# Kernel tuning notes

Measured on AMD Instinct MI355X. Metric: run time of the kernel, lower is better.

The kernel has to match this reference:

```python
import jax, jax.numpy as jnp
import numpy as np

N, E, D = 50000, 512000, 128

def mish(x):
    return x * jnp.tanh(jax.nn.softplus(x))

def ln(x, g, b):
    m = jnp.mean(x, axis=-1, keepdims=True)
    v = jnp.var(x, axis=-1, keepdims=True)
    return (x - m) / jnp.sqrt(v + 1e-5) * g + b

def setup_inputs():
    key = jax.random.key(0)
    ks = jax.random.split(key, 16)
    W = lambda k, i, o: jax.random.normal(k, (i, o), jnp.float32) * 0.02
    z = jnp.zeros((D,), jnp.float32)
    o = jnp.ones((D,), jnp.float32)
    return {
        "node_feat": jax.random.normal(ks[0], (N, D), jnp.float32),
        "coord_feat": jax.random.normal(ks[1], (N, D), jnp.float32),
        "Wq": W(ks[2], D, D), "bq": z, "gq": o, "beq": z,
        "Wk": W(ks[3], D, D), "bk": z, "gk": o, "bek": z,
        "Wm1": W(ks[4], D, D), "bm1": z, "gm": o, "bem": z,
        "Wm2": W(ks[5], D, D), "bm2": z,
        "Wb1": W(ks[6], D, D), "bb1": z, "gb": o, "beb": z,
        "Wb2": W(ks[7], D, D), "bb2": z,
        "Ww1": W(ks[8], D, D), "bw1": z, "gw": o, "bew": z,
        "Ww2": W(ks[9], D, D), "bw2": z,
        "Wn1": W(ks[10], 2 * D, D), "bn1": z,
        "Wn2": W(ks[11], D, D), "bn2": z,
        "Wc1": W(ks[12], D, D), "bc1": z,
        "Wc2": W(ks[13], D, D),
        "src": jax.random.randint(ks[14], (E,), 0, N, jnp.int32),
        "dst": jax.random.randint(ks[15], (E,), 0, N, jnp.int32),
    }

def reference(node_feat, coord_feat, Wq, bq, gq, beq, Wk, bk, gk, bek,
              Wm1, bm1, gm, bem, Wm2, bm2, Wb1, bb1, gb, beb, Wb2, bb2,
              Ww1, bw1, gw, bew, Ww2, bw2, Wn1, bn1, Wn2, bn2, Wc1, bc1, Wc2,
              src, dst):
    # linear_q / linear_k on coord features: Linear -> LayerNorm -> Mish
    q = mish(ln(coord_feat @ Wq + bq, gq, beq))   # [N, D]
    k = mish(ln(coord_feat @ Wk + bk, gk, bek))   # [N, D]
    # u_sub_v('q','k'): per-edge q[src] - k[dst]
    rel = q[src] - k[dst]                          # [E, D]
    radial = jnp.sum(rel * rel, axis=-1, keepdims=True)  # [E, 1]
    rel = rel / jnp.sqrt(radial + 1e-8)
    # relative position encodings from dst coord features
    xd = coord_feat[dst]                           # [E, D]
    pem = mish(ln(xd @ Wm1 + bm1, gm, bem)) @ Wm2 + bm2
    peb = mish(ln(xd @ Wb1 + bb1, gb, beb)) @ Wb2 + bb2
    rel = rel * pem + peb
    # weight_encoding MLP
    w = mish(ln(rel @ Ww1 + bw1, gw, bew)) @ Ww2 + bw2  # [E, D]
    # dgl.softmax_edges over a single graph: softmax across the edge axis
    w = jax.nn.softmax(w, axis=0)
    # update_all(copy_e, sum): scatter-add edge weights to destination nodes
    h_neigh = jax.ops.segment_sum(w, dst, num_segments=N)  # [N, D]
    h = mish(jnp.concatenate([node_feat, h_neigh], axis=-1) @ Wn1 + bn1) @ Wn2 + bn2
    x = mish(coord_feat @ Wc1 + bc1) @ Wc2
    return (h, x)
```

## Files before the change

kernel.cpp:

```cpp
#include <hip/hip_runtime.h>
#include <cstdint>
#include <cstddef>

#define DN 128
#define NND 50000
#define NED 512000
#define NSCAN 49

typedef __attribute__((ext_vector_type(8))) short bf8;
typedef __attribute__((ext_vector_type(4))) float f4;
typedef unsigned short us;

__device__ __forceinline__ us f2bf(float f){
  union { float f; unsigned int u; } c; c.f = f;
  unsigned int r = c.u + 0x7fffu + ((c.u >> 16) & 1u);
  return (us)(r >> 16);
}
__device__ __forceinline__ float bf2f(us u){
  union { unsigned int u; float f; } c; c.u = ((unsigned int)u) << 16;
  return c.f;
}
__device__ __forceinline__ float mishf(float x){
  float e = __expf(x);
  float u = 1.f + e;
  float u2 = u * u;
  float t = (u2 - 1.f) / (u2 + 1.f);
  return x * ((x > 20.f) ? 1.f : t);
}

#define MFMA16(a, b, c) __builtin_amdgcn_mfma_f32_16x16x32_bf16((a), (b), (c), 0, 0, 0)

__device__ __forceinline__ bf8 lds_frag(const us* base, int row, int rowStrideB, int kElem){
  int byte = row * rowStrideB + kElem * 2;
  byte ^= (row & 7) << 4;
  return *(const bf8*)((const char*)base + byte);
}
__device__ __forceinline__ bf8 gfrag(const us* W, int n, int K, int kElem){
  return *(const bf8*)(W + (size_t)n * K + kElem);
}

template<int OUT_BF16>
__device__ __forceinline__ void store_tile(void* outp, int nrows, int r0,
                                           int wr, int wc, int g, int s, int ostride,
                                           const f4 (&A)[2][4]){
#pragma unroll
  for (int rt = 0; rt < 2; ++rt)
#pragma unroll
    for (int ct = 0; ct < 4; ++ct)
#pragma unroll
      for (int reg = 0; reg < 4; ++reg){
        int row = r0 + wr*32 + rt*16 + g*4 + reg;
        if (row < nrows){
          int col = wc*64 + ct*16 + s;
          float v = A[rt][ct][reg];
          if constexpr (OUT_BF16 != 0)
            ((us*)outp)[(size_t)row*ostride + col] = f2bf(v);
          else
            ((float*)outp)[(size_t)row*ostride + col] = v;
        }
      }
}

__device__ __forceinline__ void gemm_reg(const bf8 (&a)[2][4], const us* __restrict__ WT,
                                         const float* __restrict__ bias,
                                         int wc, int g, int s, f4 (&acc)[2][4]){
#pragma unroll
  for (int ct = 0; ct < 4; ++ct){
    float bv = bias ? bias[wc*64 + ct*16 + s] : 0.f;
    f4 t = {bv, bv, bv, bv};
    acc[0][ct] = t; acc[1][ct] = t;
  }
#pragma unroll
  for (int ct = 0; ct < 4; ++ct){
    int n = wc*64 + ct*16 + s;
#pragma unroll
    for (int kk = 0; kk < 4; ++kk){
      bf8 b = gfrag(WT, n, DN, kk*32 + g*8);
      acc[0][ct] = MFMA16(a[0][kk], b, acc[0][ct]);
      acc[1][ct] = MFMA16(a[1][kk], b, acc[1][ct]);
    }
  }
}

__device__ __forceinline__ void ln_mish(f4 (&acc)[2][4],
                                        const float* __restrict__ gam,
                                        const float* __restrict__ bet,
                                        int wr, int wc, int g, int s,
                                        float (*rowsum)[64][2], float (*rowsq)[64][2],
                                        int buf){
  float gv[4], bev[4];
#pragma unroll
  for (int ct = 0; ct < 4; ++ct){ int n = wc*64 + ct*16 + s; gv[ct] = gam[n]; bev[ct] = bet[n]; }
#pragma unroll
  for (int rt = 0; rt < 2; ++rt)
#pragma unroll
    for (int reg = 0; reg < 4; ++reg){
      float sm = acc[rt][0][reg] + acc[rt][1][reg] + acc[rt][2][reg] + acc[rt][3][reg];
      float sq = acc[rt][0][reg]*acc[rt][0][reg] + acc[rt][1][reg]*acc[rt][1][reg]
               + acc[rt][2][reg]*acc[rt][2][reg] + acc[rt][3][reg]*acc[rt][3][reg];
#pragma unroll
      for (int m = 1; m < 16; m <<= 1){ sm += __shfl_xor(sm, m, 64); sq += __shfl_xor(sq, m, 64); }
      if (s == 0){
        int row = wr*32 + rt*16 + g*4 + reg;
        rowsum[buf][row][wc] = sm; rowsq[buf][row][wc] = sq;
      }
    }
  __syncthreads();
#pragma unroll
  for (int rt = 0; rt < 2; ++rt)
#pragma unroll
    for (int reg = 0; reg < 4; ++reg){
      int row = wr*32 + rt*16 + g*4 + reg;
      float sm = rowsum[buf][row][0] + rowsum[buf][row][1];
      float sq = rowsq[buf][row][0] + rowsq[buf][row][1];
      float mu = sm * (1.f/128.f);
      float var = sq * (1.f/128.f) - mu*mu;
      float rs = rsqrtf(var + 1e-5f);
#pragma unroll
      for (int ct = 0; ct < 4; ++ct)
        acc[rt][ct][reg] = mishf((acc[rt][ct][reg] - mu) * rs * gv[ct] + bev[ct]);
    }
}

__device__ __forceinline__ void write_T(us* Tsh, int wr, int wc, int g, int s,
                                        const f4 (&A)[2][4]){
#pragma unroll
  for (int rt = 0; rt < 2; ++rt)
#pragma unroll
    for (int ct = 0; ct < 4; ++ct)
#pragma unroll
      for (int reg = 0; reg < 4; ++reg){
        int row = wr*32 + rt*16 + g*4 + reg;
        int col = wc*64 + ct*16 + s;
        int byte = row*256 + col*2; byte ^= (row & 7) << 4;
        *(us*)((char*)Tsh + byte) = f2bf(A[rt][ct][reg]);
      }
}

__device__ __forceinline__ void load_a2(const us* Tsh, int wr, int g, int s, bf8 (&a2)[2][4]){
#pragma unroll
  for (int rt = 0; rt < 2; ++rt)
#pragma unroll
    for (int kk = 0; kk < 4; ++kk)
      a2[rt][kk] = lds_frag(Tsh, wr*32 + rt*16 + s, 256, kk*32 + g*8);
}

__global__ __launch_bounds__(256, 2)
void node_fused(const float* __restrict__ X,
                const us* __restrict__ WqT,  const float* __restrict__ bq,
                const float* __restrict__ gq, const float* __restrict__ beq,
                const us* __restrict__ WkT,  const float* __restrict__ bk,
                const float* __restrict__ gk, const float* __restrict__ bek,
                const us* __restrict__ Wm1T, const float* __restrict__ bm1,
                const float* __restrict__ gm, const float* __restrict__ bem,
                const us* __restrict__ Wm2T, const float* __restrict__ bm2,
                const us* __restrict__ Wb1T, const float* __restrict__ bb1,
                const float* __restrict__ gb, const float* __restrict__ beb,
                const us* __restrict__ Wb2T, const float* __restrict__ bb2,
                const us* __restrict__ Wc1T, const float* __restrict__ bc1,
                const us* __restrict__ Wc2T,
                us* __restrict__ qt, us* __restrict__ kmb, float* __restrict__ xout)
{
  __shared__ us Ash[64 * DN];
  __shared__ float rowsum[2][64][2];
  __shared__ float rowsq[2][64][2];

  const int tid = threadIdx.x;
  const int r0 = blockIdx.x * 64;

  {
    int r = tid >> 2, c4 = tid & 3;
    int grow = r0 + r; if (grow >= NND) grow = NND - 1;
    const f4* sp = (const f4*)(X + (size_t)grow * DN + c4 * 32);
#pragma unroll
    for (int j = 0; j < 4; ++j){
      f4 v0 = sp[2*j], v1 = sp[2*j+1];
      bf8 o;
#pragma unroll
      for (int q = 0; q < 4; ++q){ o[q] = (short)f2bf(v0[q]); o[4+q] = (short)f2bf(v1[q]); }
      int byte = r*256 + c4*64 + j*16; byte ^= (r & 7) << 4;
      *(bf8*)((char*)Ash + byte) = o;
    }
  }
  __syncthreads();

  const int lane = tid & 63, w = tid >> 6;
  const int wr = w >> 1, wc = w & 1;
  const int g = lane >> 4, s = lane & 15;

  bf8 a[2][4];
#pragma unroll
  for (int rt = 0; rt < 2; ++rt)
#pragma unroll
    for (int kk = 0; kk < 4; ++kk)
      a[rt][kk] = lds_frag(Ash, wr*32 + rt*16 + s, 256, kk*32 + g*8);
  __syncthreads();

  f4 acc[2][4], acc2[2][4];
  bf8 a2[2][4];

  gemm_reg(a, WqT, bq, wc, g, s, acc);
  ln_mish(acc, gq, beq, wr, wc, g, s, rowsum, rowsq, 0);
  store_tile<1>((void*)qt, NND, r0, wr, wc, g, s, DN, acc);

  gemm_reg(a, WkT, bk, wc, g, s, acc);
  ln_mish(acc, gk, bek, wr, wc, g, s, rowsum, rowsq, 1);
  store_tile<1>((void*)kmb, NND, r0, wr, wc, g, s, 384, acc);

  gemm_reg(a, Wm1T, bm1, wc, g, s, acc);
  ln_mish(acc, gm, bem, wr, wc, g, s, rowsum, rowsq, 0);
  write_T(Ash, wr, wc, g, s, acc);
  __syncthreads();
  load_a2(Ash, wr, g, s, a2);
#pragma unroll
  for (int ct = 0; ct < 4; ++ct){
    float bv = bm2[wc*64 + ct*16 + s]; f4 t = {bv,bv,bv,bv}; acc2[0][ct] = t; acc2[1][ct] = t;
  }
#pragma unroll
  for (int ct = 0; ct < 4; ++ct){
    int n = wc*64 + ct*16 + s;
#pragma unroll
    for (int kk = 0; kk < 4; ++kk){
      bf8 b = gfrag(Wm2T, n, DN, kk*32 + g*8);
      acc2[0][ct] = MFMA16(a2[0][kk], b, acc2[0][ct]);
      acc2[1][ct] = MFMA16(a2[1][kk], b, acc2[1][ct]);
    }
  }
  store_tile<1>((void*)(kmb + 128), NND, r0, wr, wc, g, s, 384, acc2);

  gemm_reg(a, Wb1T, bb1, wc, g, s, acc);
  ln_mish(acc, gb, beb, wr, wc, g, s, rowsum, rowsq, 1);
  write_T(Ash, wr, wc, g, s, acc);
  __syncthreads();
  load_a2(Ash, wr, g, s, a2);
#pragma unroll
  for (int ct = 0; ct < 4; ++ct){
    float bv = bb2[wc*64 + ct*16 + s]; f4 t = {bv,bv,bv,bv}; acc2[0][ct] = t; acc2[1][ct] = t;
  }
#pragma unroll
  for (int ct = 0; ct < 4; ++ct){
    int n = wc*64 + ct*16 + s;
#pragma unroll
    for (int kk = 0; kk < 4; ++kk){
      bf8 b = gfrag(Wb2T, n, DN, kk*32 + g*8);
      acc2[0][ct] = MFMA16(a2[0][kk], b, acc2[0][ct]);
      acc2[1][ct] = MFMA16(a2[1][kk], b, acc2[1][ct]);
    }
  }
  store_tile<1>((void*)(kmb + 256), NND, r0, wr, wc, g, s, 384, acc2);

  gemm_reg(a, Wc1T, bc1, wc, g, s, acc);
#pragma unroll
  for (int rt = 0; rt < 2; ++rt)
#pragma unroll
    for (int ct = 0; ct < 4; ++ct)
#pragma unroll
      for (int reg = 0; reg < 4; ++reg)
        acc[rt][ct][reg] = mishf(acc[rt][ct][reg]);
  __syncthreads();
  write_T(Ash, wr, wc, g, s, acc);
  __syncthreads();
  load_a2(Ash, wr, g, s, a2);
#pragma unroll
  for (int ct = 0; ct < 4; ++ct){ f4 t = {0,0,0,0}; acc2[0][ct] = t; acc2[1][ct] = t; }
#pragma unroll
  for (int ct = 0; ct < 4; ++ct){
    int n = wc*64 + ct*16 + s;
#pragma unroll
    for (int kk = 0; kk < 4; ++kk){
      bf8 b = gfrag(Wc2T, n, DN, kk*32 + g*8);
      acc2[0][ct] = MFMA16(a2[0][kk], b, acc2[0][ct]);
      acc2[1][ct] = MFMA16(a2[1][kk], b, acc2[1][ct]);
    }
  }
  store_tile<0>((void*)xout, NND, r0, wr, wc, g, s, DN, acc2);
}

__global__ void csr_count(const int* __restrict__ dst, int* __restrict__ deg){
  int e = blockIdx.x * 256 + threadIdx.x;
  if (e < NED) atomicAdd(&deg[dst[e]], 1);
}

__global__ __launch_bounds__(1024) void csr_blocksum(const int* __restrict__ deg,
                                                     int* __restrict__ bsum){
  __shared__ int sb[1024];
  int t = threadIdx.x, idx = blockIdx.x * 1024 + t;
  sb[t] = (idx < NND) ? deg[idx] : 0;
  __syncthreads();
  for (int off = 512; off > 0; off >>= 1){
    if (t < off) sb[t] += sb[t + off];
    __syncthreads();
  }
  if (t == 0) bsum[blockIdx.x] = sb[0];
}

__global__ void csr_scanroot(const int* __restrict__ bsum, int* __restrict__ boff){
  if (threadIdx.x == 0){
    int run = 0;
    for (int b = 0; b < NSCAN; ++b){ boff[b] = run; run += bsum[b]; }
  }
}

__global__ __launch_bounds__(1024) void csr_scatter(const int* __restrict__ deg,
                                                    const int* __restrict__ boff,
                                                    int* __restrict__ fillctr){
  __shared__ int ss[1024];
  int t = threadIdx.x, idx = blockIdx.x * 1024 + t;
  int v = (idx < NND) ? deg[idx] : 0;
  ss[t] = v;
  __syncthreads();
  for (int off = 1; off < 1024; off <<= 1){
    int x = (t >= off) ? ss[t - off] : 0;
    __syncthreads();
    ss[t] += x;
    __syncthreads();
  }
  if (idx < NND){
    int p = boff[blockIdx.x] + ss[t] - v;
    fillctr[idx] = p;
  }
}

__global__ void csr_fill(const int* __restrict__ src, const int* __restrict__ dst,
                         int* __restrict__ fillctr,
                         int* __restrict__ ssorted, int* __restrict__ dsorted){
  int e = blockIdx.x * 256 + threadIdx.x;
  if (e < NED){
    int d = dst[e];
    int p = atomicAdd(&fillctr[d], 1);
    ssorted[p] = src[e];
    dsorted[p] = d;
  }
}

__global__ __launch_bounds__(256, 2)
void edge_kernel(const us* __restrict__ qtab,
                 const us* __restrict__ kmb,
                 const us* __restrict__ W1T,
                 const us* __restrict__ W2T,
                 const float* __restrict__ bw1,
                 const float* __restrict__ gwp,
                 const float* __restrict__ bewp,
                 const float* __restrict__ bw2,
                 const int* __restrict__ ssorted,
                 const int* __restrict__ dsorted,
                 float* __restrict__ hacc,
                 float* __restrict__ colsum8)
{
  __shared__ us Ash[64 * DN];
  __shared__ float rowsum[1][64][2];
  __shared__ float rowsq[1][64][2];
  __shared__ int dsh[64];

  const int tid = threadIdx.x;
  const int nchunk = gridDim.x >> 3;
  const int swz = (blockIdx.x & 7) * nchunk + (blockIdx.x >> 3);
  const int e0 = swz * 64;
  const int lane = tid & 63, w = tid >> 6;
  const int wr = w >> 1, wc = w & 1;
  const int g = lane >> 4, s = lane & 15;

  if (tid < 64) dsh[tid] = dsorted[e0 + tid];

  bf8 B1[4][4], B2[4][4];
  float b1v[4], gv[4], bev[4], b2v[4];
#pragma unroll
  for (int ct = 0; ct < 4; ++ct){
    int n = wc*64 + ct*16 + s;
#pragma unroll
    for (int kk = 0; kk < 4; ++kk){
      B1[ct][kk] = gfrag(W1T, n, DN, kk*32 + g*8);
      B2[ct][kk] = gfrag(W2T, n, DN, kk*32 + g*8);
    }
    b1v[ct] = bw1[n]; gv[ct] = gwp[n]; bev[ct] = bewp[n]; b2v[ct] = bw2[n];
  }

  {
    int r = tid >> 2, c4 = tid & 3;
    int e = e0 + r;
    int sn = ssorted[e], dn = dsorted[e];
    const bf8* qp = (const bf8*)(qtab + (size_t)sn * DN + c4 * 32);
    const us* kb = kmb + (size_t)dn * 384 + c4 * 32;
    float rel[32]; float ss = 0.f;
#pragma unroll
    for (int j = 0; j < 4; ++j){
      bf8 qv = qp[j];
      bf8 kv = *(const bf8*)(kb + j*8);
#pragma unroll
      for (int q = 0; q < 8; ++q){
        float d = bf2f((us)qv[q]) - bf2f((us)kv[q]);
        rel[j*8+q] = d; ss += d * d;
      }
    }
    ss += __shfl_xor(ss, 1, 64);
    ss += __shfl_xor(ss, 2, 64);
    float rinv = rsqrtf(ss + 1e-8f);
#pragma unroll
    for (int j = 0; j < 4; ++j){
      bf8 mv = *(const bf8*)(kb + 128 + j*8);
      bf8 bv = *(const bf8*)(kb + 256 + j*8);
      bf8 o;
#pragma unroll
      for (int q = 0; q < 8; ++q){
        float v = rel[j*8+q] * rinv * bf2f((us)mv[q]) + bf2f((us)bv[q]);
        o[q] = (short)f2bf(v);
      }
      int byte = r*256 + c4*64 + j*16; byte ^= (r & 7) << 4;
      *(bf8*)((char*)Ash + byte) = o;
    }
  }
  __syncthreads();

  f4 acc[2][4];
#pragma unroll
  for (int ct = 0; ct < 4; ++ct){ f4 t = {b1v[ct], b1v[ct], b1v[ct], b1v[ct]}; acc[0][ct] = t; acc[1][ct] = t; }
  bf8 a[2][4];
#pragma unroll
  for (int rt = 0; rt < 2; ++rt)
#pragma unroll
    for (int kk = 0; kk < 4; ++kk)
      a[rt][kk] = lds_frag(Ash, wr*32 + rt*16 + s, 256, kk*32 + g*8);
#pragma unroll
  for (int ct = 0; ct < 4; ++ct)
#pragma unroll
    for (int kk = 0; kk < 4; ++kk){
      acc[0][ct] = MFMA16(a[0][kk], B1[ct][kk], acc[0][ct]);
      acc[1][ct] = MFMA16(a[1][kk], B1[ct][kk], acc[1][ct]);
    }

#pragma unroll
  for (int rt = 0; rt < 2; ++rt)
#pragma unroll
    for (int reg = 0; reg < 4; ++reg){
      float sm = acc[rt][0][reg] + acc[rt][1][reg] + acc[rt][2][reg] + acc[rt][3][reg];
      float sq = acc[rt][0][reg]*acc[rt][0][reg] + acc[rt][1][reg]*acc[rt][1][reg]
               + acc[rt][2][reg]*acc[rt][2][reg] + acc[rt][3][reg]*acc[rt][3][reg];
#pragma unroll
      for (int m = 1; m < 16; m <<= 1){ sm += __shfl_xor(sm, m, 64); sq += __shfl_xor(sq, m, 64); }
      if (s == 0){
        int row = wr*32 + rt*16 + g*4 + reg;
        rowsum[0][row][wc] = sm; rowsq[0][row][wc] = sq;
      }
    }
  __syncthreads();
#pragma unroll
  for (int rt = 0; rt < 2; ++rt)
#pragma unroll
    for (int reg = 0; reg < 4; ++reg){
      int row = wr*32 + rt*16 + g*4 + reg;
      float sm = rowsum[0][row][0] + rowsum[0][row][1];
      float sq = rowsq[0][row][0] + rowsq[0][row][1];
      float mu = sm * (1.f/128.f);
      float var = sq * (1.f/128.f) - mu*mu;
      float rs = rsqrtf(var + 1e-5f);
#pragma unroll
      for (int ct = 0; ct < 4; ++ct)
        acc[rt][ct][reg] = mishf((acc[rt][ct][reg] - mu) * rs * gv[ct] + bev[ct]);
    }

  write_T(Ash, wr, wc, g, s, acc);
  __syncthreads();

  f4 p[2][4];
#pragma unroll
  for (int ct = 0; ct < 4; ++ct){ f4 t = {b2v[ct], b2v[ct], b2v[ct], b2v[ct]}; p[0][ct] = t; p[1][ct] = t; }
  bf8 a2[2][4];
  load_a2(Ash, wr, g, s, a2);
#pragma unroll
  for (int ct = 0; ct < 4; ++ct)
#pragma unroll
    for (int kk = 0; kk < 4; ++kk){
      p[0][ct] = MFMA16(a2[0][kk], B2[ct][kk], p[0][ct]);
      p[1][ct] = MFMA16(a2[1][kk], B2[ct][kk], p[1][ct]);
    }
#pragma unroll
  for (int rt = 0; rt < 2; ++rt)
#pragma unroll
    for (int ct = 0; ct < 4; ++ct)
#pragma unroll
      for (int reg = 0; reg < 4; ++reg)
        p[rt][ct][reg] = __expf(p[rt][ct][reg]);

  __syncthreads();

  write_T(Ash, wr, wc, g, s, p);
  __syncthreads();

  {
    int col = tid & 127, half = tid >> 7;
    int rbeg = half * 32;
    float csum = 0.f;
    int prev = dsh[rbeg];
    float run = 0.f;
#pragma unroll 8
    for (int r = rbeg; r < rbeg + 32; ++r){
      int d = dsh[r];
      int byte = r*256 + col*2; byte ^= (r & 7) << 4;
      float v = bf2f(*(const us*)((const char*)Ash + byte));
      csum += v;
      if (d != prev){
        atomicAdd(&hacc[(size_t)prev * DN + col], run);
        run = v; prev = d;
      } else {
        run += v;
      }
    }
    atomicAdd(&hacc[(size_t)prev * DN + col], run);
    atomicAdd(&colsum8[(blockIdx.x & 7) * DN + col], csum);
  }
}

__global__ __launch_bounds__(256, 2)
void final_h(const float* __restrict__ nodef,
             const float* __restrict__ hacc,
             const float* __restrict__ colsum8,
             const us* __restrict__ Wn1T,
             const float* __restrict__ bn1,
             const us* __restrict__ Wn2T,
             const float* __restrict__ bn2,
             float* __restrict__ outh)
{
  __shared__ us Ash[64 * 256];
  __shared__ float rcs[DN];

  const int tid = threadIdx.x;
  const int r0 = blockIdx.x * 64;

  if (tid < DN){
    float ssum = 0.f;
#pragma unroll
    for (int x = 0; x < 8; ++x) ssum += colsum8[x * DN + tid];
    rcs[tid] = 1.f / ssum;
  }
  __syncthreads();

  {
    int r = tid >> 2, c4 = tid & 3;
    int grow = r0 + r; if (grow >= NND) grow = NND - 1;
    const f4* np = (const f4*)(nodef + (size_t)grow * DN + c4 * 32);
    const f4* hp = (const f4*)(hacc + (size_t)grow * DN + c4 * 32);
#pragma unroll
    for (int j = 0; j < 4; ++j){
      f4 v0 = np[2*j], v1 = np[2*j+1];
      bf8 o;
#pragma unroll
      for (int q = 0; q < 4; ++q){ o[q] = (short)f2bf(v0[q]); o[4+q] = (short)f2bf(v1[q]); }
      int byte = r*512 + c4*64 + j*16; byte ^= (r & 7) << 4;
      *(bf8*)((char*)Ash + byte) = o;
      f4 h0 = hp[2*j], h1 = hp[2*j+1];
      bf8 o2;
#pragma unroll
      for (int q = 0; q < 4; ++q){
        o2[q]   = (short)f2bf(h0[q] * rcs[c4*32 + j*8 + q]);
        o2[4+q] = (short)f2bf(h1[q] * rcs[c4*32 + j*8 + 4 + q]);
      }
      int byte2 = r*512 + 256 + c4*64 + j*16; byte2 ^= (r & 7) << 4;
      *(bf8*)((char*)Ash + byte2) = o2;
    }
  }
  __syncthreads();

  const int lane = tid & 63, w = tid >> 6;
  const int wr = w >> 1, wc = w & 1;
  const int g = lane >> 4, s = lane & 15;

  float b1v[4], b2v[4];
#pragma unroll
  for (int ct = 0; ct < 4; ++ct){ int n = wc*64 + ct*16 + s; b1v[ct] = bn1[n]; b2v[ct] = bn2[n]; }

  f4 acc[2][4];
#pragma unroll
  for (int ct = 0; ct < 4; ++ct){ f4 t = {b1v[ct], b1v[ct], b1v[ct], b1v[ct]}; acc[0][ct] = t; acc[1][ct] = t; }

  bf8 a[2][8];
#pragma unroll
  for (int rt = 0; rt < 2; ++rt)
#pragma unroll
    for (int kk = 0; kk < 8; ++kk)
      a[rt][kk] = lds_frag(Ash, wr*32 + rt*16 + s, 512, kk*32 + g*8);
  __syncthreads();

#pragma unroll
  for (int ct = 0; ct < 4; ++ct){
    int n = wc*64 + ct*16 + s;
#pragma unroll
    for (int kk = 0; kk < 8; ++kk){
      bf8 b = gfrag(Wn1T, n, 256, kk*32 + g*8);
      acc[0][ct] = MFMA16(a[0][kk], b, acc[0][ct]);
      acc[1][ct] = MFMA16(a[1][kk], b, acc[1][ct]);
    }
  }

#pragma unroll
  for (int rt = 0; rt < 2; ++rt)
#pragma unroll
    for (int ct = 0; ct < 4; ++ct)
#pragma unroll
      for (int reg = 0; reg < 4; ++reg)
        acc[rt][ct][reg] = mishf(acc[rt][ct][reg]);
  write_T((us*)Ash, wr, wc, g, s, acc);
  __syncthreads();

  f4 acc2[2][4];
#pragma unroll
  for (int ct = 0; ct < 4; ++ct){ f4 t = {b2v[ct], b2v[ct], b2v[ct], b2v[ct]}; acc2[0][ct] = t; acc2[1][ct] = t; }
  bf8 a2[2][4];
  load_a2((const us*)Ash, wr, g, s, a2);
#pragma unroll
  for (int ct = 0; ct < 4; ++ct){
    int n = wc*64 + ct*16 + s;
#pragma unroll
    for (int kk = 0; kk < 4; ++kk){
      bf8 b = gfrag(Wn2T, n, DN, kk*32 + g*8);
      acc2[0][ct] = MFMA16(a2[0][kk], b, acc2[0][ct]);
      acc2[1][ct] = MFMA16(a2[1][kk], b, acc2[1][ct]);
    }
  }
  store_tile<0>((void*)outh, NND, r0, wr, wc, g, s, DN, acc2);
}

struct WPrepArgs {
  const float* w[12];
  us* wt[12];
  int K[12];
};

__global__ void prep_weights(WPrepArgs a){
  int widx = blockIdx.y;
  int K = a.K[widx];
  int idx = blockIdx.x * 256 + threadIdx.x;
  if (idx >= DN * K) return;
  int kshift = (K == 256) ? 8 : 7;
  int n = idx >> kshift;
  int k = idx & (K - 1);
  a.wt[widx][idx] = f2bf(a.w[widx][(size_t)k * DN + n]);
}

extern "C" void kernel_launch(void* const* d_in, const int* in_sizes, int n_in,
                              void* d_out, int out_size, void* d_ws, size_t ws_size,
                              hipStream_t stream) {
  const float* node_feat = (const float*)d_in[0];
  const float* coordf    = (const float*)d_in[1];
  const float* Wq  = (const float*)d_in[2];
  const float* bq  = (const float*)d_in[3];
  const float* gq  = (const float*)d_in[4];
  const float* beq = (const float*)d_in[5];
  const float* Wk  = (const float*)d_in[6];
  const float* bk  = (const float*)d_in[7];
  const float* gk  = (const float*)d_in[8];
  const float* bek = (const float*)d_in[9];
  const float* Wm1 = (const float*)d_in[10];
  const float* bm1 = (const float*)d_in[11];
  const float* gm  = (const float*)d_in[12];
  const float* bem = (const float*)d_in[13];
  const float* Wm2 = (const float*)d_in[14];
  const float* bm2 = (const float*)d_in[15];
  const float* Wb1 = (const float*)d_in[16];
  const float* bb1 = (const float*)d_in[17];
  const float* gb  = (const float*)d_in[18];
  const float* beb = (const float*)d_in[19];
  const float* Wb2 = (const float*)d_in[20];
  const float* bb2 = (const float*)d_in[21];
  const float* Ww1 = (const float*)d_in[22];
  const float* bw1 = (const float*)d_in[23];
  const float* gw  = (const float*)d_in[24];
  const float* bew = (const float*)d_in[25];
  const float* Ww2 = (const float*)d_in[26];
  const float* bw2 = (const float*)d_in[27];
  const float* Wn1 = (const float*)d_in[28];
  const float* bn1 = (const float*)d_in[29];
  const float* Wn2 = (const float*)d_in[30];
  const float* bn2 = (const float*)d_in[31];
  const float* Wc1 = (const float*)d_in[32];
  const float* bc1 = (const float*)d_in[33];
  const float* Wc2 = (const float*)d_in[34];
  const int* srcI  = (const int*)d_in[35];
  const int* dstI  = (const int*)d_in[36];

  char* ws = (char*)d_ws;
  size_t off = 0;
  auto alloc = [&](size_t bytes) -> char* {
    char* p = ws + off;
    off += (bytes + 255) & ~(size_t)255;
    return p;
  };
  us*    qt      = (us*)alloc((size_t)NND * DN * 2);
  us*    kmb     = (us*)alloc((size_t)NND * 384 * 2);
  float* hacc    = (float*)alloc((size_t)NND * DN * 4);
  float* colsum8 = (float*)alloc(8 * DN * 4);
  int*   deg     = (int*)alloc((size_t)NND * 4);
  int*   fillctr = (int*)alloc((size_t)NND * 4);
  int*   ssorted = (int*)alloc((size_t)NED * 4);
  int*   dsorted = (int*)alloc((size_t)NED * 4);
  int*   bsum    = (int*)alloc((size_t)NSCAN * 4);
  int*   boff    = (int*)alloc((size_t)NSCAN * 4);
  us*    wtb     = (us*)alloc((size_t)12 * 16384 * 2);

  hipMemsetAsync(hacc, 0, (size_t)NND * DN * 4 + 8 * DN * 4, stream);
  hipMemsetAsync(deg, 0, (size_t)NND * 4, stream);

  WPrepArgs pa;
  const float* wsrc[12] = {Wq, Wk, Wm1, Wm2, Wb1, Wb2, Ww1, Ww2, Wc1, Wc2, Wn2, Wn1};
  for (int i = 0; i < 12; ++i){
    pa.w[i] = wsrc[i];
    pa.wt[i] = wtb + (size_t)i * 16384;
    pa.K[i] = (i == 11) ? 256 : 128;
  }
  prep_weights<<<dim3(128, 12), 256, 0, stream>>>(pa);

  csr_count<<<(NED + 255) / 256, 256, 0, stream>>>(dstI, deg);
  csr_blocksum<<<NSCAN, 1024, 0, stream>>>(deg, bsum);
  csr_scanroot<<<1, 64, 0, stream>>>(bsum, boff);
  csr_scatter<<<NSCAN, 1024, 0, stream>>>(deg, boff, fillctr);
  csr_fill<<<(NED + 255) / 256, 256, 0, stream>>>(srcI, dstI, fillctr, ssorted, dsorted);

  const int NB = (NND + 63) / 64;

  node_fused<<<NB, 256, 0, stream>>>(coordf,
      pa.wt[0], bq, gq, beq,
      pa.wt[1], bk, gk, bek,
      pa.wt[2], bm1, gm, bem, pa.wt[3], bm2,
      pa.wt[4], bb1, gb, beb, pa.wt[5], bb2,
      pa.wt[8], bc1, pa.wt[9],
      qt, kmb, (float*)d_out + (size_t)NND * DN);

  edge_kernel<<<NED / 64, 256, 0, stream>>>(qt, kmb, pa.wt[6], pa.wt[7],
                                            bw1, gw, bew, bw2, ssorted, dsorted,
                                            hacc, colsum8);

  final_h<<<NB, 256, 0, stream>>>(node_feat, hacc, colsum8,
                                  pa.wt[11], bn1, pa.wt[10], bn2, (float*)d_out);
}
```

Measured before the change: 517.1 us.

## Give each warp its own 16-edge tile to drop block-wide syncs in edge kernel

The edge kernel is restructured so each of the four waves handles 16 edges end to end, with full 128-column GEMMs, a per-wave LayerNorm via shuffles, and a private LDS tile. This removes the cross-wave row-statistics exchange and most __syncthreads barriers. Weight fragments are now streamed from global/L2 inside the GEMM rather than preloaded into registers, which trades register pressure for repeated weight loads per wave. The gathers for q, k, pem and peb are also issued up front to overlap memory latency.

```diff
diff --git a/kernel.cpp b/kernel.cpp
--- a/kernel.cpp
+++ b/kernel.cpp
@@ -143,6 +143,65 @@
 #pragma unroll
     for (int kk = 0; kk < 4; ++kk)
       a2[rt][kk] = lds_frag(Tsh, wr*32 + rt*16 + s, 256, kk*32 + g*8);
+}
+
+__device__ __forceinline__ void loadA16(const us* T, int g, int s, bf8 (&a)[4]){
+#pragma unroll
+  for (int kk = 0; kk < 4; ++kk)
+    a[kk] = lds_frag(T, s, 256, kk*32 + g*8);
+}
+
+__device__ __forceinline__ void gemm8(const bf8 (&a)[4], const us* __restrict__ WT,
+                                      const float* __restrict__ bias,
+                                      int g, int s, f4 (&acc)[8]){
+#pragma unroll
+  for (int ct = 0; ct < 8; ++ct){
+    float bv = bias ? bias[ct*16 + s] : 0.f;
+    f4 t = {bv, bv, bv, bv};
+    acc[ct] = t;
+  }
+#pragma unroll
+  for (int ct = 0; ct < 8; ++ct){
+    int n = ct*16 + s;
+#pragma unroll
+    for (int kk = 0; kk < 4; ++kk)
+      acc[ct] = MFMA16(a[kk], gfrag(WT, n, DN, kk*32 + g*8), acc[ct]);
+  }
+}
+
+__device__ __forceinline__ void ln_mish8(f4 (&acc)[8],
+                                         const float* __restrict__ gam,
+                                         const float* __restrict__ bet, int s){
+  float mu[4], rs[4];
+#pragma unroll
+  for (int reg = 0; reg < 4; ++reg){
+    float sm = 0.f, sq = 0.f;
+#pragma unroll
+    for (int ct = 0; ct < 8; ++ct){ float v = acc[ct][reg]; sm += v; sq += v*v; }
+#pragma unroll
+    for (int m = 1; m < 16; m <<= 1){ sm += __shfl_xor(sm, m, 64); sq += __shfl_xor(sq, m, 64); }
+    float mm = sm * (1.f/128.f);
+    float var = sq * (1.f/128.f) - mm*mm;
+    mu[reg] = mm; rs[reg] = rsqrtf(var + 1e-5f);
+  }
+#pragma unroll
+  for (int ct = 0; ct < 8; ++ct){
+    float gv = gam[ct*16 + s], bv = bet[ct*16 + s];
+#pragma unroll
+    for (int reg = 0; reg < 4; ++reg)
+      acc[ct][reg] = mishf((acc[ct][reg] - mu[reg]) * rs[reg] * gv + bv);
+  }
+}
+
+__device__ __forceinline__ void writeT16(us* T, int g, int s, const f4 (&A)[8]){
+#pragma unroll
+  for (int ct = 0; ct < 8; ++ct)
+#pragma unroll
+    for (int reg = 0; reg < 4; ++reg){
+      int row = g*4 + reg, col = ct*16 + s;
+      int byte = row*256 + col*2; byte ^= (row & 7) << 4;
+      *(us*)((char*)T + byte) = f2bf(A[ct][reg]);
+    }
 }
 
 __global__ __launch_bounds__(256, 2)
@@ -347,143 +406,75 @@
                  float* __restrict__ hacc,
                  float* __restrict__ colsum8)
 {
-  __shared__ us Ash[64 * DN];
-  __shared__ float rowsum[1][64][2];
-  __shared__ float rowsq[1][64][2];
+  __shared__ us Tsh[4][16 * DN];
   __shared__ int dsh[64];
 
   const int tid = threadIdx.x;
+  const int lane = tid & 63, w = tid >> 6;
+  const int g = lane >> 4, s = lane & 15;
+  const int r = lane >> 2, c4 = lane & 3;
+
   const int nchunk = gridDim.x >> 3;
   const int swz = (blockIdx.x & 7) * nchunk + (blockIdx.x >> 3);
-  const int e0 = swz * 64;
-  const int lane = tid & 63, w = tid >> 6;
-  const int wr = w >> 1, wc = w & 1;
-  const int g = lane >> 4, s = lane & 15;
-
-  if (tid < 64) dsh[tid] = dsorted[e0 + tid];
-
-  bf8 B1[4][4], B2[4][4];
-  float b1v[4], gv[4], bev[4], b2v[4];
-#pragma unroll
-  for (int ct = 0; ct < 4; ++ct){
-    int n = wc*64 + ct*16 + s;
-#pragma unroll
-    for (int kk = 0; kk < 4; ++kk){
-      B1[ct][kk] = gfrag(W1T, n, DN, kk*32 + g*8);
-      B2[ct][kk] = gfrag(W2T, n, DN, kk*32 + g*8);
-    }
-    b1v[ct] = bw1[n]; gv[ct] = gwp[n]; bev[ct] = bewp[n]; b2v[ct] = bw2[n];
-  }
-
-  {
-    int r = tid >> 2, c4 = tid & 3;
-    int e = e0 + r;
-    int sn = ssorted[e], dn = dsorted[e];
-    const bf8* qp = (const bf8*)(qtab + (size_t)sn * DN + c4 * 32);
-    const us* kb = kmb + (size_t)dn * 384 + c4 * 32;
-    float rel[32]; float ss = 0.f;
-#pragma unroll
-    for (int j = 0; j < 4; ++j){
-      bf8 qv = qp[j];
-      bf8 kv = *(const bf8*)(kb + j*8);
-#pragma unroll
-      for (int q = 0; q < 8; ++q){
-        float d = bf2f((us)qv[q]) - bf2f((us)kv[q]);
-        rel[j*8+q] = d; ss += d * d;
-      }
-    }
-    ss += __shfl_xor(ss, 1, 64);
-    ss += __shfl_xor(ss, 2, 64);
-    float rinv = rsqrtf(ss + 1e-8f);
-#pragma unroll
-    for (int j = 0; j < 4; ++j){
-      bf8 mv = *(const bf8*)(kb + 128 + j*8);
-      bf8 bv = *(const bf8*)(kb + 256 + j*8);
-      bf8 o;
-#pragma unroll
-      for (int q = 0; q < 8; ++q){
-        float v = rel[j*8+q] * rinv * bf2f((us)mv[q]) + bf2f((us)bv[q]);
-        o[q] = (short)f2bf(v);
-      }
-      int byte = r*256 + c4*64 + j*16; byte ^= (r & 7) << 4;
-      *(bf8*)((char*)Ash + byte) = o;
-    }
-  }
-  __syncthreads();
-
-  f4 acc[2][4];
-#pragma unroll
-  for (int ct = 0; ct < 4; ++ct){ f4 t = {b1v[ct], b1v[ct], b1v[ct], b1v[ct]}; acc[0][ct] = t; acc[1][ct] = t; }
-  bf8 a[2][4];
-#pragma unroll
-  for (int rt = 0; rt < 2; ++rt)
-#pragma unroll
-    for (int kk = 0; kk < 4; ++kk)
-      a[rt][kk] = lds_frag(Ash, wr*32 + rt*16 + s, 256, kk*32 + g*8);
-#pragma unroll
-  for (int ct = 0; ct < 4; ++ct)
-#pragma unroll
-    for (int kk = 0; kk < 4; ++kk){
-      acc[0][ct] = MFMA16(a[0][kk], B1[ct][kk], acc[0][ct]);
-      acc[1][ct] = MFMA16(a[1][kk], B1[ct][kk], acc[1][ct]);
-    }
-
-#pragma unroll
-  for (int rt = 0; rt < 2; ++rt)
-#pragma unroll
-    for (int reg = 0; reg < 4; ++reg){
-      float sm = acc[rt][0][reg] + acc[rt][1][reg] + acc[rt][2][reg] + acc[rt][3][reg];
-      float sq = acc[rt][0][reg]*acc[rt][0][reg] + acc[rt][1][reg]*acc[rt][1][reg]
-               + acc[rt][2][reg]*acc[rt][2][reg] + acc[rt][3][reg]*acc[rt][3][reg];
-#pragma unroll
-      for (int m = 1; m < 16; m <<= 1){ sm += __shfl_xor(sm, m, 64); sq += __shfl_xor(sq, m, 64); }
-      if (s == 0){
-        int row = wr*32 + rt*16 + g*4 + reg;
-        rowsum[0][row][wc] = sm; rowsq[0][row][wc] = sq;
-      }
-    }
-  __syncthreads();
-#pragma unroll
-  for (int rt = 0; rt < 2; ++rt)
-#pragma unroll
-    for (int reg = 0; reg < 4; ++reg){
-      int row = wr*32 + rt*16 + g*4 + reg;
-      float sm = rowsum[0][row][0] + rowsum[0][row][1];
-      float sq = rowsq[0][row][0] + rowsq[0][row][1];
-      float mu = sm * (1.f/128.f);
-      float var = sq * (1.f/128.f) - mu*mu;
-      float rs = rsqrtf(var + 1e-5f);
-#pragma unroll
-      for (int ct = 0; ct < 4; ++ct)
-        acc[rt][ct][reg] = mishf((acc[rt][ct][reg] - mu) * rs * gv[ct] + bev[ct]);
-    }
-
-  write_T(Ash, wr, wc, g, s, acc);
-  __syncthreads();
-
-  f4 p[2][4];
-#pragma unroll
-  for (int ct = 0; ct < 4; ++ct){ f4 t = {b2v[ct], b2v[ct], b2v[ct], b2v[ct]}; p[0][ct] = t; p[1][ct] = t; }
-  bf8 a2[2][4];
-  load_a2(Ash, wr, g, s, a2);
-#pragma unroll
-  for (int ct = 0; ct < 4; ++ct)
-#pragma unroll
-    for (int kk = 0; kk < 4; ++kk){
-      p[0][ct] = MFMA16(a2[0][kk], B2[ct][kk], p[0][ct]);
-      p[1][ct] = MFMA16(a2[1][kk], B2[ct][kk], p[1][ct]);
-    }
-#pragma unroll
-  for (int rt = 0; rt < 2; ++rt)
-#pragma unroll
-    for (int ct = 0; ct < 4; ++ct)
-#pragma unroll
-      for (int reg = 0; reg < 4; ++reg)
-        p[rt][ct][reg] = __expf(p[rt][ct][reg]);
-
-  __syncthreads();
-
-  write_T(Ash, wr, wc, g, s, p);
+  const int e0 = swz * 64 + w * 16;
+  us* T = (us*)Tsh[w];
+
+  const int e = e0 + r;
+  const int sn = ssorted[e], dn = dsorted[e];
+  const bf8* qp = (const bf8*)(qtab + (size_t)sn * DN + c4 * 32);
+  const us*  kb = kmb + (size_t)dn * 384 + c4 * 32;
+  bf8 qv[4], kv[4], mv[4], bv[4];
+#pragma unroll
+  for (int j = 0; j < 4; ++j){
+    qv[j] = qp[j];
+    kv[j] = *(const bf8*)(kb + j*8);
+    mv[j] = *(const bf8*)(kb + 128 + j*8);
+    bv[j] = *(const bf8*)(kb + 256 + j*8);
+  }
+  if (c4 == 0) dsh[w*16 + r] = dn;
+
+  float ss = 0.f;
+#pragma unroll
+  for (int j = 0; j < 4; ++j)
+#pragma unroll
+    for (int q = 0; q < 8; ++q){
+      float d = bf2f((us)qv[j][q]) - bf2f((us)kv[j][q]);
+      ss += d * d;
+    }
+  ss += __shfl_xor(ss, 1, 64);
+  ss += __shfl_xor(ss, 2, 64);
+  float rinv = rsqrtf(ss + 1e-8f);
+
+#pragma unroll
+  for (int j = 0; j < 4; ++j){
+    bf8 o;
+#pragma unroll
+    for (int q = 0; q < 8; ++q){
+      float d = bf2f((us)qv[j][q]) - bf2f((us)kv[j][q]);
+      float v = d * rinv * bf2f((us)mv[j][q]) + bf2f((us)bv[j][q]);
+      o[q] = (short)f2bf(v);
+    }
+    int byte = r*256 + c4*64 + j*16; byte ^= (r & 7) << 4;
+    *(bf8*)((char*)T + byte) = o;
+  }
+
+  bf8 a[4];
+  loadA16(T, g, s, a);
+  f4 acc[8];
+  gemm8(a, W1T, bw1, g, s, acc);
+  ln_mish8(acc, gwp, bewp, s);
+  writeT16(T, g, s, acc);
+  bf8 a2[4];
+  loadA16(T, g, s, a2);
+  f4 p[8];
+  gemm8(a2, W2T, bw2, g, s, p);
+#pragma unroll
+  for (int ct = 0; ct < 8; ++ct)
+#pragma unroll
+    for (int reg = 0; reg < 4; ++reg)
+      p[ct][reg] = __expf(p[ct][reg]);
+
+  writeT16(T, g, s, p);
   __syncthreads();
 
   {
@@ -493,10 +484,11 @@
     int prev = dsh[rbeg];
     float run = 0.f;
 #pragma unroll 8
-    for (int r = rbeg; r < rbeg + 32; ++r){
-      int d = dsh[r];
-      int byte = r*256 + col*2; byte ^= (r & 7) << 4;
-      float v = bf2f(*(const us*)((const char*)Ash + byte));
+    for (int r2 = rbeg; r2 < rbeg + 32; ++r2){
+      int qw = r2 >> 4, lr = r2 & 15;
+      int byte = lr*256 + col*2; byte ^= (lr & 7) << 4;
+      float v = bf2f(*(const us*)((const char*)Tsh[qw] + byte));
+      int d = dsh[r2];
       csum += v;
       if (d != prev){
         atomicAdd(&hacc[(size_t)prev * DN + col], run);
```

After: 558.3 us. 8.0% more time.
